# Performance work log

Hardware: AMD Instinct MI355X
Metric: run time of the kernel (lower is better)

The kernel has to match this reference:

```python
import jax, jax.numpy as jnp
import numpy as np

N = 4096     # num nodes
FEAT = 500   # knn attribute dim
HID = 512    # args.hid_dim
E = 65536    # edges (avg degree 16)
T = 8        # args.time -> euler steps with step_size=1


def setup_inputs() -> dict:
    key = jax.random.key(0)
    ks = jax.random.split(key, 10)
    knn = jax.random.normal(ks[0], (N, FEAT), jnp.float32)
    adj = jax.random.uniform(ks[1], (N, N), jnp.float32)
    norm_factor = jnp.ones((), jnp.float32)
    edge_index = jax.random.randint(ks[2], (2, E), 0, N, dtype=jnp.int32).astype(jnp.int64)
    edge_weight = jax.random.uniform(ks[3], (E,), jnp.float32)
    # AGCN params (init eye + small noise so math is non-trivial)
    w1 = jnp.eye(N, dtype=jnp.float32) + 0.01 * jax.random.normal(ks[4], (N, N), jnp.float32)
    w2 = jnp.eye(N, dtype=jnp.float32) + 0.01 * jax.random.normal(ks[5], (N, N), jnp.float32)
    # extractor: Linear(N, HID) then Linear(HID, HID), kaiming-normal (relu), zero bias
    W0 = jax.random.normal(ks[6], (HID, N), jnp.float32) * np.float32((2.0 / N) ** 0.5)
    b0 = jnp.zeros((HID,), jnp.float32)
    W1 = jax.random.normal(ks[7], (HID, HID), jnp.float32) * np.float32((2.0 / HID) ** 0.5)
    b1 = jnp.zeros((HID,), jnp.float32)
    # LaplacianODEFunc scalar params
    alpha_train = jnp.asarray(0.5, jnp.float32)
    beta_train = jnp.asarray(0.1, jnp.float32)
    return dict(knn=knn, adj=adj, norm_factor=norm_factor, w1=w1, w2=w2,
                W0=W0, b0=b0, W1=W1, b1=b1, edge_weight=edge_weight,
                alpha_train=alpha_train, beta_train=beta_train, edge_index=edge_index)


def _spmm(edge_index, edge_weight, x):
    # out[row] += w * x[col], row=edge_index[0], col=edge_index[1]
    msg = edge_weight[:, None] * x[edge_index[1]]          # [E, HID]
    return jax.ops.segment_sum(msg, edge_index[0], num_segments=x.shape[0])


def reference(knn, adj, norm_factor, w1, w2, W0, b0, W1, b1,
              edge_weight, alpha_train, beta_train, edge_index):
    # ---- AGCN ----
    H = (adj @ w1) @ adj.T                                  # [N, N]
    H = (H @ w2) @ knn                                      # [N, FEAT]
    embed = H @ H.T                                         # [N, N]
    norm = jnp.maximum(jnp.linalg.norm(embed, axis=1, keepdims=True), 1e-12)
    embed = embed / norm                                    # F.normalize(dim=1)
    # ---- extractor MLP (no activation in source; dropout=eval no-op) ----
    h = embed @ W0.T + b0                                   # [N, HID]
    h = h @ W1.T + b1                                       # [N, HID]
    # ---- ODE diffusion: dx/dt = sigmoid(a)*(Ax - x) + b*x0, explicit Euler dt=1 ----
    x0 = jax.lax.stop_gradient(h)
    alpha = jax.nn.sigmoid(alpha_train)

    def step(x, _):
        ax = _spmm(edge_index, edge_weight, x)
        return x + alpha * (ax - x) + beta_train * x0, None

    z_ode, _ = jax.lax.scan(step, h, None, length=T)
    z = jax.nn.relu(norm_factor * z_ode + h)
    z = (z - z.mean(0)) / jnp.std(z, ddof=1)                # torch std is unbiased
    return z
```

## Files before the change

kernel.cpp:

```cpp
#include <hip/hip_runtime.h>
#include <stdint.h>
#include <stddef.h>

typedef __bf16 bf16;
typedef __attribute__((ext_vector_type(8))) __bf16 bf16x8;
typedef __attribute__((ext_vector_type(4))) __bf16 bf16x4;
typedef __attribute__((ext_vector_type(4))) float f32x4;

#define NN 4096
#define HIDD 512
#define NE 65536

__device__ inline void gll16(const void* g, void* l) {
    __builtin_amdgcn_global_load_lds(
        (const __attribute__((address_space(1))) void*)g,
        (__attribute__((address_space(3))) void*)l, 16, 0, 0);
}

__global__ void cvt_f32_bf16(const float* __restrict__ in, bf16* __restrict__ out, int n) {
    int i = (blockIdx.x * 256 + threadIdx.x) * 4;
    if (i >= n) return;
    float4 v = *reinterpret_cast<const float4*>(in + i);
    bf16x4 o;
    o[0] = (bf16)v.x; o[1] = (bf16)v.y; o[2] = (bf16)v.z; o[3] = (bf16)v.w;
    *reinterpret_cast<bf16x4*>(out + i) = o;
}

__global__ void reduce_bf16_slices(const bf16* __restrict__ in, bf16* __restrict__ out,
                                   int n, int S) {
    int i = (blockIdx.x * 256 + threadIdx.x) * 8;
    if (i >= n) return;
    float acc[8] = {};
    for (int k = 0; k < S; ++k) {
        bf16x8 v = *reinterpret_cast<const bf16x8*>(in + (size_t)k * n + i);
#pragma unroll
        for (int j = 0; j < 8; ++j) acc[j] += (float)v[j];
    }
    bf16x8 o;
#pragma unroll
    for (int j = 0; j < 8; ++j) o[j] = (bf16)acc[j];
    *reinterpret_cast<bf16x8*>(out + i) = o;
}

__global__ void transpose_pad_f32(const float* __restrict__ in, bf16* __restrict__ out,
                                  int R, int C, int Cpad) {
    __shared__ bf16 tile[32][33];
    int c0 = blockIdx.x * 32, r0 = blockIdx.y * 32;
    int tx = threadIdx.x, ty = threadIdx.y;
    for (int i = ty; i < 32; i += 8) {
        int r = r0 + i, c = c0 + tx;
        bf16 v = (bf16)0.f;
        if (r < R && c < C) v = (bf16)in[(size_t)r * C + c];
        tile[i][tx] = v;
    }
    __syncthreads();
    for (int i = ty; i < 32; i += 8) {
        int oc = c0 + i, orow = r0 + tx;
        if (oc < Cpad && orow < R) out[(size_t)oc * R + orow] = tile[tx][i];
    }
}

__global__ void transpose_bf16(const bf16* __restrict__ in, bf16* __restrict__ out,
                               int R, int C) {
    __shared__ bf16 tile[32][33];
    int c0 = blockIdx.x * 32, r0 = blockIdx.y * 32;
    int tx = threadIdx.x, ty = threadIdx.y;
    for (int i = ty; i < 32; i += 8)
        tile[i][tx] = in[(size_t)(r0 + i) * C + c0 + tx];
    __syncthreads();
    for (int i = ty; i < 32; i += 8)
        out[(size_t)(c0 + i) * R + r0 + tx] = tile[tx][i];
}

template<int OMODE, bool HAS_BIAS, bool ROW_SCALE>
__global__ __launch_bounds__(256)
void gemm_nt(const bf16* __restrict__ A, const bf16* __restrict__ B,
             void* __restrict__ Cp, const float* __restrict__ bias,
             const float* __restrict__ rowscale, int M, int N, int K) {
    __shared__ __align__(16) bf16 As[128 * 32];
    __shared__ __align__(16) bf16 Bs[128 * 32];
    const int tid  = threadIdx.x;
    const int wave = tid >> 6;
    const int lane = tid & 63;
    const int m0 = blockIdx.y * 128, n0 = blockIdx.x * 128;
    const int lrow = lane >> 2;
    const int lcol = (lane & 3) * 8;
    const int c0 = wave * 2;
    const size_t arow0 = (size_t)(m0 + c0 * 16 + lrow) * K + lcol;
    const size_t arow1 = (size_t)(m0 + (c0 + 1) * 16 + lrow) * K + lcol;
    const size_t brow0 = (size_t)(n0 + c0 * 16 + lrow) * K + lcol;
    const size_t brow1 = (size_t)(n0 + (c0 + 1) * 16 + lrow) * K + lcol;
    bf16* asd0 = &As[c0 * 512];
    bf16* asd1 = &As[(c0 + 1) * 512];
    bf16* bsd0 = &Bs[c0 * 512];
    bf16* bsd1 = &Bs[(c0 + 1) * 512];

    f32x4 acc[4][4] = {};

    const int wm = (wave >> 1) * 64;
    const int wn = (wave & 1) * 64;
    const int fm = wm + (lane & 15);
    const int fn = wn + (lane & 15);
    const int fk = (lane >> 4) * 8;

    const int kper = K / gridDim.z;
    const int kz0 = blockIdx.z * kper;
    const int kz1 = kz0 + kper;

    for (int k0 = kz0; k0 < kz1; k0 += 32) {
        gll16(A + arow0 + k0, asd0);
        gll16(A + arow1 + k0, asd1);
        gll16(B + brow0 + k0, bsd0);
        gll16(B + brow1 + k0, bsd1);
        __syncthreads();
        bf16x8 af[4], bg[4];
#pragma unroll
        for (int i = 0; i < 4; ++i)
            af[i] = *reinterpret_cast<const bf16x8*>(&As[(fm + i * 16) * 32 + fk]);
#pragma unroll
        for (int j = 0; j < 4; ++j)
            bg[j] = *reinterpret_cast<const bf16x8*>(&Bs[(fn + j * 16) * 32 + fk]);
#pragma unroll
        for (int i = 0; i < 4; ++i)
#pragma unroll
            for (int j = 0; j < 4; ++j)
                acc[i][j] = __builtin_amdgcn_mfma_f32_16x16x32_bf16(af[i], bg[j], acc[i][j], 0, 0, 0);
        __syncthreads();
    }

    const int rbase = m0 + wm + (lane >> 4) * 4;
    const int cbase = n0 + wn + (lane & 15);
    float* outf = (float*)Cp + (size_t)blockIdx.z * M * N;
    bf16*  outb = (bf16*)Cp;
    bf16*  outp = (bf16*)Cp + (size_t)blockIdx.z * M * N;
#pragma unroll
    for (int i = 0; i < 4; ++i) {
#pragma unroll
        for (int j = 0; j < 4; ++j) {
            int col = cbase + j * 16;
            float bv = 0.f;
            if (HAS_BIAS) bv = bias[col];
#pragma unroll
            for (int r = 0; r < 4; ++r) {
                int row = rbase + i * 16 + r;
                float v = acc[i][j][r];
                if (ROW_SCALE) v *= rowscale[row];
                v += bv;
                if (OMODE == 0)      outf[(size_t)row * N + col] = v;
                else if (OMODE == 1) outb[(size_t)row * N + col] = (bf16)v;
                else                 outp[(size_t)row * N + col] = (bf16)v;
            }
        }
    }
}

__global__ void colnorm_part(const bf16* __restrict__ Ht, const float* __restrict__ Rf,
                             float* __restrict__ n2) {
    int i = blockIdx.x * 128 + threadIdx.x;
    int a0 = blockIdx.y * 64;
    float s = 0.f;
    for (int a = a0; a < a0 + 64; ++a)
        s += Rf[(size_t)a * NN + i] * (float)Ht[(size_t)a * NN + i];
    atomicAdd(&n2[i], s);
}

__global__ void colnorm_fin(const float* __restrict__ n2, float* __restrict__ inv) {
    int i = blockIdx.x * 256 + threadIdx.x;
    inv[i] = 1.f / fmaxf(sqrtf(n2[i]), 1e-12f);
}

__global__ void csr_count(const int* __restrict__ ei, int* __restrict__ cnt, int E) {
    int e = blockIdx.x * 256 + threadIdx.x;
    if (e < E) atomicAdd(&cnt[ei[e]], 1);
}

__global__ void scan_4096(const int* __restrict__ cnt, int* __restrict__ rs) {
    __shared__ int s[1024];
    int t = threadIdx.x;
    int b = t * 4;
    int a0 = cnt[b], a1 = cnt[b + 1], a2 = cnt[b + 2], a3 = cnt[b + 3];
    int tot = a0 + a1 + a2 + a3;
    s[t] = tot;
    __syncthreads();
    for (int off = 1; off < 1024; off <<= 1) {
        int v = (t >= off) ? s[t - off] : 0;
        __syncthreads();
        s[t] += v;
        __syncthreads();
    }
    int excl = s[t] - tot;
    rs[b] = excl; rs[b + 1] = excl + a0; rs[b + 2] = excl + a0 + a1; rs[b + 3] = excl + a0 + a1 + a2;
    if (t == 1023) rs[4096] = s[1023];
}

__global__ void csr_scatter(const int* __restrict__ ei, const float* __restrict__ ew,
                            int* __restrict__ cur, int* __restrict__ ccol,
                            float* __restrict__ cw, int E) {
    int e = blockIdx.x * 256 + threadIdx.x;
    if (e < E) {
        int r = ei[e];
        int p = atomicAdd(&cur[r], 1);
        ccol[p] = ei[E + e];
        cw[p] = ew[e];
    }
}

__global__ void ode_step_bf16(const bf16* __restrict__ xin, const bf16* __restrict__ x0,
                              bf16* __restrict__ xout, const int* __restrict__ rs,
                              const int* __restrict__ ccol, const float* __restrict__ cw,
                              const float* __restrict__ alpha_p, const float* __restrict__ beta_p) {
    int row = blockIdx.x * 4 + (threadIdx.x >> 6);
    int lane = threadIdx.x & 63;
    float alpha = 1.f / (1.f + expf(-alpha_p[0]));
    float beta = beta_p[0];
    const bf16x8* xin8 = (const bf16x8*)xin;
    float acc[8] = {};
    int p0 = rs[row], p1 = rs[row + 1];
    for (int p = p0; p < p1; ++p) {
        int c = ccol[p]; float w = cw[p];
        bf16x8 v = xin8[(size_t)c * 64 + lane];
#pragma unroll
        for (int j = 0; j < 8; ++j) acc[j] += w * (float)v[j];
    }
    bf16x8 xi = xin8[(size_t)row * 64 + lane];
    bf16x8 xz = ((const bf16x8*)x0)[(size_t)row * 64 + lane];
    bf16x8 r;
#pragma unroll
    for (int j = 0; j < 8; ++j) {
        float x = (float)xi[j];
        r[j] = (bf16)(x + alpha * (acc[j] - x) + beta * (float)xz[j]);
    }
    ((bf16x8*)xout)[(size_t)row * 64 + lane] = r;
}

__global__ void epi1(const bf16* __restrict__ x8, const bf16* __restrict__ h,
                     const float* __restrict__ nf_p, float* __restrict__ z,
                     float* __restrict__ colsum, float* __restrict__ gst) {
    __shared__ float r1[512], r2[512];
    int b = blockIdx.x, j = threadIdx.x;
    float nf = nf_p[0];
    float cp = 0.f, sq = 0.f;
    for (int i = 0; i < 8; ++i) {
        size_t idx = (size_t)(b * 8 + i) * HIDD + j;
        float v = nf * (float)x8[idx] + (float)h[idx];
        v = fmaxf(v, 0.f);
        z[idx] = v;
        cp += v; sq += v * v;
    }
    atomicAdd(&colsum[j], cp);
    r1[j] = cp; r2[j] = sq;
    __syncthreads();
    for (int off = 256; off > 0; off >>= 1) {
        if (j < off) { r1[j] += r1[j + off]; r2[j] += r2[j + off]; }
        __syncthreads();
    }
    if (j == 0) { atomicAdd(&gst[0], r1[0]); atomicAdd(&gst[1], r2[0]); }
}

__global__ void epi2(const float* __restrict__ z, const float* __restrict__ colsum,
                     const float* __restrict__ gst, float* __restrict__ out) {
    size_t idx = (size_t)blockIdx.x * 256 + threadIdx.x;
    int j = (int)(idx & (HIDD - 1));
    float n = (float)NN * (float)HIDD;
    float gmean = gst[0] / n;
    float var = (gst[1] - n * gmean * gmean) / (n - 1.f);
    float istd = rsqrtf(var);
    float mean = colsum[j] * (1.f / (float)NN);
    out[idx] = (z[idx] - mean) * istd;
}

extern "C" void kernel_launch(void* const* d_in, const int* in_sizes, int n_in,
                              void* d_out, int out_size, void* d_ws, size_t ws_size,
                              hipStream_t stream) {
    const float* knn  = (const float*)d_in[0];
    const float* adj  = (const float*)d_in[1];
    const float* nf   = (const float*)d_in[2];
    const float* w1   = (const float*)d_in[3];
    const float* w2   = (const float*)d_in[4];
    const float* W0   = (const float*)d_in[5];
    const float* b0   = (const float*)d_in[6];
    const float* W1   = (const float*)d_in[7];
    const float* b1   = (const float*)d_in[8];
    const float* ew   = (const float*)d_in[9];
    const float* alph = (const float*)d_in[10];
    const float* beta = (const float*)d_in[11];
    const int*   ei   = (const int*)d_in[12];

    char* w = (char*)d_ws;
    size_t off = 0;
    auto alloc = [&](size_t bytes) -> char* {
        char* p = w + off;
        off += (bytes + 255) & ~(size_t)255;
        return p;
    };
    const size_t SZ_NN  = (size_t)NN * NN * sizeof(bf16);
    const size_t SZ_TH  = (size_t)HIDD * NN * sizeof(bf16);
    bf16* Bar  = (bf16*)alloc(SZ_NN);
    bf16* Car  = (bf16*)alloc(SZ_NN);
    bf16* knnT = (bf16*)alloc(SZ_TH);
    bf16* tA   = (bf16*)alloc(SZ_TH);
    bf16* tB   = (bf16*)alloc(SZ_TH);
    float* tf  = (float*)alloc((size_t)16 * 1024 * 1024);
    bf16* Hm   = (bf16*)alloc(SZ_TH);
    bf16* Gb   = (bf16*)alloc((size_t)HIDD * HIDD * sizeof(bf16));
    bf16* M0tb = (bf16*)alloc((size_t)HIDD * HIDD * sizeof(bf16));
    bf16* h1b  = (bf16*)alloc((size_t)NN * HIDD * sizeof(bf16));
    bf16* hb   = (bf16*)alloc((size_t)NN * HIDD * sizeof(bf16));
    float* inv = (float*)alloc(NN * sizeof(float));
    float* n2  = (float*)alloc(NN * sizeof(float));
    int*  cnt  = (int*)alloc(NN * sizeof(int));
    int*  rs   = (int*)alloc((NN + 1) * sizeof(int));
    int*  cur  = (int*)alloc(NN * sizeof(int));
    int*  ccol = (int*)alloc(NE * sizeof(int));
    float* cw  = (float*)alloc(NE * sizeof(float));
    float* colsum = (float*)alloc(HIDD * sizeof(float));
    float* gst = (float*)alloc(2 * sizeof(float));
    bf16* tfb = (bf16*)tf;
    bf16* W1b = (bf16*)((char*)Car + 16 * 1024 * 1024);
    bf16* xA  = (bf16*)Car;
    bf16* xB  = (bf16*)Car + (size_t)NN * HIDD;
    (void)ws_size; (void)n_in; (void)in_sizes; (void)out_size;

    dim3 tb(32, 8);
    const int nTH = HIDD * NN;
    const int nHH = HIDD * HIDD;

    transpose_pad_f32<<<dim3(16, 128), tb, 0, stream>>>(knn, knnT, NN, 500, HIDD);
    cvt_f32_bf16<<<(NN * NN) / 1024, 256, 0, stream>>>(w2, Car, NN * NN);
    transpose_pad_f32<<<dim3(128, 128), tb, 0, stream>>>(adj, Bar, NN, NN, NN);

    gemm_nt<2, false, false><<<dim3(32, 4, 4), 256, 0, stream>>>(knnT, Car, tfb, nullptr, nullptr, HIDD, NN, NN);
    reduce_bf16_slices<<<nTH / 2048, 256, 0, stream>>>(tfb, tA, nTH, 4);
    gemm_nt<2, false, false><<<dim3(32, 4, 4), 256, 0, stream>>>(tA, Bar, tfb, nullptr, nullptr, HIDD, NN, NN);
    reduce_bf16_slices<<<nTH / 2048, 256, 0, stream>>>(tfb, tB, nTH, 4);
    cvt_f32_bf16<<<(NN * NN) / 1024, 256, 0, stream>>>(w1, Car, NN * NN);
    gemm_nt<2, false, false><<<dim3(32, 4, 4), 256, 0, stream>>>(tB, Car, tfb, nullptr, nullptr, HIDD, NN, NN);
    reduce_bf16_slices<<<nTH / 2048, 256, 0, stream>>>(tfb, tA, nTH, 4);
    cvt_f32_bf16<<<(NN * NN) / 1024, 256, 0, stream>>>(adj, Bar, NN * NN);
    gemm_nt<2, false, false><<<dim3(32, 4, 4), 256, 0, stream>>>(tA, Bar, tfb, nullptr, nullptr, HIDD, NN, NN);
    reduce_bf16_slices<<<nTH / 2048, 256, 0, stream>>>(tfb, tB, nTH, 4);

    transpose_bf16<<<dim3(128, 16), tb, 0, stream>>>(tB, Hm, HIDD, NN);

    gemm_nt<2, false, false><<<dim3(4, 4, 16), 256, 0, stream>>>(tB, tB, tfb, nullptr, nullptr, HIDD, HIDD, NN);
    reduce_bf16_slices<<<nHH / 2048, 256, 0, stream>>>(tfb, Gb, nHH, 16);

    gemm_nt<0, false, false><<<dim3(32, 4, 1), 256, 0, stream>>>(Gb, Hm, tf, nullptr, nullptr, HIDD, NN, HIDD);
    hipMemsetAsync(n2, 0, NN * sizeof(float), stream);
    colnorm_part<<<dim3(32, 8), 128, 0, stream>>>(tB, tf, n2);
    colnorm_fin<<<NN / 256, 256, 0, stream>>>(n2, inv);

    cvt_f32_bf16<<<(HIDD * NN) / 1024, 256, 0, stream>>>(W0, Car, HIDD * NN);
    gemm_nt<2, false, false><<<dim3(4, 4, 16), 256, 0, stream>>>(Car, tB, tfb, nullptr, nullptr, HIDD, HIDD, NN);
    reduce_bf16_slices<<<nHH / 2048, 256, 0, stream>>>(tfb, M0tb, nHH, 16);

    gemm_nt<1, true, true><<<dim3(4, 32, 1), 256, 0, stream>>>(Hm, M0tb, h1b, b0, inv, NN, HIDD, HIDD);
    cvt_f32_bf16<<<(HIDD * HIDD) / 1024, 256, 0, stream>>>(W1, W1b, HIDD * HIDD);
    gemm_nt<1, true, false><<<dim3(4, 32, 1), 256, 0, stream>>>(h1b, W1b, hb, b1, nullptr, NN, HIDD, HIDD);

    hipMemsetAsync(cnt, 0, NN * sizeof(int), stream);
    csr_count<<<NE / 256, 256, 0, stream>>>(ei, cnt, NE);
    scan_4096<<<1, 1024, 0, stream>>>(cnt, rs);
    hipMemcpyAsync(cur, rs, NN * sizeof(int), hipMemcpyDeviceToDevice, stream);
    csr_scatter<<<NE / 256, 256, 0, stream>>>(ei, ew, cur, ccol, cw, NE);

    const bf16* xi = hb;
    bf16* xo = xA;
    for (int s = 0; s < 8; ++s) {
        ode_step_bf16<<<NN / 4, 256, 0, stream>>>(xi, hb, xo, rs, ccol, cw, alph, beta);
        xi = xo;
        xo = (s % 2 == 0) ? xB : xA;
    }

    hipMemsetAsync(colsum, 0, HIDD * sizeof(float), stream);
    hipMemsetAsync(gst, 0, 2 * sizeof(float), stream);
    epi1<<<NN / 8, 512, 0, stream>>>(xB, hb, nf, tf, colsum, gst);
    epi2<<<(NN * HIDD) / 256, 256, 0, stream>>>(tf, colsum, gst, (float*)d_out);
}
```

Before: 676.0 us.

## Fold extractor weights into one GEMM, raise split-K, dual-output adj conversion

The transposed and plain bf16 copies of adj are now produced in a single pass, so the second fp32 conversion of adj is gone. Split-K depth is doubled for the large and Gram GEMMs, and the K=512 GEMMs are split into two slices. The two extractor linear layers are pre-multiplied into one 512x512 matrix (W1·M0) with a fused bias b1+W1·b0, which replaces one NxHID GEMM with a small HIDxHID GEMM. In exchange it adds more partial-sum traffic, extra reduce passes and an additional bf16 rounding of the combined weight.

```diff
diff --git a/kernel.cpp b/kernel.cpp
--- a/kernel.cpp
+++ b/kernel.cpp
@@ -58,6 +58,22 @@
         int oc = c0 + i, orow = r0 + tx;
         if (oc < Cpad && orow < R) out[(size_t)oc * R + orow] = tile[tx][i];
     }
+}
+
+__global__ void transpose_dual_f32(const float* __restrict__ in, bf16* __restrict__ outT,
+                                   bf16* __restrict__ outD, int Nn) {
+    __shared__ bf16 tile[32][33];
+    int c0 = blockIdx.x * 32, r0 = blockIdx.y * 32;
+    int tx = threadIdx.x, ty = threadIdx.y;
+    for (int i = ty; i < 32; i += 8) {
+        int r = r0 + i, c = c0 + tx;
+        bf16 v = (bf16)in[(size_t)r * Nn + c];
+        tile[i][tx] = v;
+        outD[(size_t)r * Nn + c] = v;
+    }
+    __syncthreads();
+    for (int i = ty; i < 32; i += 8)
+        outT[(size_t)(c0 + i) * Nn + r0 + tx] = tile[tx][i];
 }
 
 __global__ void transpose_bf16(const bf16* __restrict__ in, bf16* __restrict__ out,
@@ -158,15 +174,50 @@
                              float* __restrict__ n2) {
     int i = blockIdx.x * 128 + threadIdx.x;
     int a0 = blockIdx.y * 64;
+    const float* Rf2 = Rf + (size_t)HIDD * NN;
     float s = 0.f;
-    for (int a = a0; a < a0 + 64; ++a)
-        s += Rf[(size_t)a * NN + i] * (float)Ht[(size_t)a * NN + i];
+    for (int a = a0; a < a0 + 64; ++a) {
+        size_t idx = (size_t)a * NN + i;
+        s += (Rf[idx] + Rf2[idx]) * (float)Ht[idx];
+    }
     atomicAdd(&n2[i], s);
 }
 
 __global__ void colnorm_fin(const float* __restrict__ n2, float* __restrict__ inv) {
     int i = blockIdx.x * 256 + threadIdx.x;
     inv[i] = 1.f / fmaxf(sqrtf(n2[i]), 1e-12f);
+}
+
+__global__ void bias_fuse(const float* __restrict__ W1, const float* __restrict__ b0,
+                          const float* __restrict__ b1, float* __restrict__ bp) {
+    int row = blockIdx.x * 4 + (threadIdx.x >> 6);
+    int lane = threadIdx.x & 63;
+    const float4* wr = (const float4*)(W1 + (size_t)row * HIDD);
+    const float4* bz = (const float4*)b0;
+    float s = 0.f;
+#pragma unroll
+    for (int j = 0; j < 2; ++j) {
+        float4 a = wr[lane * 2 + j], b = bz[lane * 2 + j];
+        s += a.x * b.x + a.y * b.y + a.z * b.z + a.w * b.w;
+    }
+    for (int off = 32; off; off >>= 1) s += __shfl_down(s, off);
+    if (lane == 0) bp[row] = b1[row] + s;
+}
+
+__global__ void reduce2_scale_bias(const bf16* __restrict__ p, bf16* __restrict__ out,
+                                   const float* __restrict__ inv, const float* __restrict__ bp) {
+    int i = (blockIdx.x * 256 + threadIdx.x) * 8;
+    const int n = NN * HIDD;
+    bf16x8 a = *reinterpret_cast<const bf16x8*>(p + i);
+    bf16x8 b = *reinterpret_cast<const bf16x8*>(p + n + i);
+    int row = i >> 9;
+    int col = i & (HIDD - 1);
+    float sc = inv[row];
+    bf16x8 o;
+#pragma unroll
+    for (int j = 0; j < 8; ++j)
+        o[j] = (bf16)(((float)a[j] + (float)b[j]) * sc + bp[col + j]);
+    *reinterpret_cast<bf16x8*>(out + i) = o;
 }
 
 __global__ void csr_count(const int* __restrict__ ei, int* __restrict__ cnt, int E) {
@@ -297,14 +348,15 @@
     const size_t SZ_TH  = (size_t)HIDD * NN * sizeof(bf16);
     bf16* Bar  = (bf16*)alloc(SZ_NN);
     bf16* Car  = (bf16*)alloc(SZ_NN);
+    bf16* Adjb = (bf16*)alloc(SZ_NN);
     bf16* knnT = (bf16*)alloc(SZ_TH);
     bf16* tA   = (bf16*)alloc(SZ_TH);
     bf16* tB   = (bf16*)alloc(SZ_TH);
-    float* tf  = (float*)alloc((size_t)16 * 1024 * 1024);
+    float* tf  = (float*)alloc((size_t)32 * 1024 * 1024);
     bf16* Hm   = (bf16*)alloc(SZ_TH);
     bf16* Gb   = (bf16*)alloc((size_t)HIDD * HIDD * sizeof(bf16));
-    bf16* M0tb = (bf16*)alloc((size_t)HIDD * HIDD * sizeof(bf16));
-    bf16* h1b  = (bf16*)alloc((size_t)NN * HIDD * sizeof(bf16));
+    bf16* M0b  = (bf16*)alloc((size_t)HIDD * HIDD * sizeof(bf16));
+    bf16* Qtb  = (bf16*)alloc((size_t)HIDD * HIDD * sizeof(bf16));
     bf16* hb   = (bf16*)alloc((size_t)NN * HIDD * sizeof(bf16));
     float* inv = (float*)alloc(NN * sizeof(float));
     float* n2  = (float*)alloc(NN * sizeof(float));
@@ -315,6 +367,7 @@
     float* cw  = (float*)alloc(NE * sizeof(float));
     float* colsum = (float*)alloc(HIDD * sizeof(float));
     float* gst = (float*)alloc(2 * sizeof(float));
+    float* bp  = (float*)alloc(HIDD * sizeof(float));
     bf16* tfb = (bf16*)tf;
     bf16* W1b = (bf16*)((char*)Car + 16 * 1024 * 1024);
     bf16* xA  = (bf16*)Car;
@@ -327,36 +380,40 @@
 
     transpose_pad_f32<<<dim3(16, 128), tb, 0, stream>>>(knn, knnT, NN, 500, HIDD);
     cvt_f32_bf16<<<(NN * NN) / 1024, 256, 0, stream>>>(w2, Car, NN * NN);
-    transpose_pad_f32<<<dim3(128, 128), tb, 0, stream>>>(adj, Bar, NN, NN, NN);
-
-    gemm_nt<2, false, false><<<dim3(32, 4, 4), 256, 0, stream>>>(knnT, Car, tfb, nullptr, nullptr, HIDD, NN, NN);
-    reduce_bf16_slices<<<nTH / 2048, 256, 0, stream>>>(tfb, tA, nTH, 4);
-    gemm_nt<2, false, false><<<dim3(32, 4, 4), 256, 0, stream>>>(tA, Bar, tfb, nullptr, nullptr, HIDD, NN, NN);
-    reduce_bf16_slices<<<nTH / 2048, 256, 0, stream>>>(tfb, tB, nTH, 4);
+    transpose_dual_f32<<<dim3(128, 128), tb, 0, stream>>>(adj, Bar, Adjb, NN);
+
+    gemm_nt<2, false, false><<<dim3(32, 4, 8), 256, 0, stream>>>(knnT, Car, tfb, nullptr, nullptr, HIDD, NN, NN);
+    reduce_bf16_slices<<<nTH / 2048, 256, 0, stream>>>(tfb, tA, nTH, 8);
+    gemm_nt<2, false, false><<<dim3(32, 4, 8), 256, 0, stream>>>(tA, Bar, tfb, nullptr, nullptr, HIDD, NN, NN);
+    reduce_bf16_slices<<<nTH / 2048, 256, 0, stream>>>(tfb, tB, nTH, 8);
     cvt_f32_bf16<<<(NN * NN) / 1024, 256, 0, stream>>>(w1, Car, NN * NN);
-    gemm_nt<2, false, false><<<dim3(32, 4, 4), 256, 0, stream>>>(tB, Car, tfb, nullptr, nullptr, HIDD, NN, NN);
-    reduce_bf16_slices<<<nTH / 2048, 256, 0, stream>>>(tfb, tA, nTH, 4);
-    cvt_f32_bf16<<<(NN * NN) / 1024, 256, 0, stream>>>(adj, Bar, NN * NN);
-    gemm_nt<2, false, false><<<dim3(32, 4, 4), 256, 0, stream>>>(tA, Bar, tfb, nullptr, nullptr, HIDD, NN, NN);
-    reduce_bf16_slices<<<nTH / 2048, 256, 0, stream>>>(tfb, tB, nTH, 4);
+    gemm_nt<2, false, false><<<dim3(32, 4, 8), 256, 0, stream>>>(tB, Car, tfb, nullptr, nullptr, HIDD, NN, NN);
+    reduce_bf16_slices<<<nTH / 2048, 256, 0, stream>>>(tfb, tA, nTH, 8);
+    gemm_nt<2, false, false><<<dim3(32, 4, 8), 256, 0, stream>>>(tA, Adjb, tfb, nullptr, nullptr, HIDD, NN, NN);
+    reduce_bf16_slices<<<nTH / 2048, 256, 0, stream>>>(tfb, tB, nTH, 8);
 
     transpose_bf16<<<dim3(128, 16), tb, 0, stream>>>(tB, Hm, HIDD, NN);
 
-    gemm_nt<2, false, false><<<dim3(4, 4, 16), 256, 0, stream>>>(tB, tB, tfb, nullptr, nullptr, HIDD, HIDD, NN);
-    reduce_bf16_slices<<<nHH / 2048, 256, 0, stream>>>(tfb, Gb, nHH, 16);
-
-    gemm_nt<0, false, false><<<dim3(32, 4, 1), 256, 0, stream>>>(Gb, Hm, tf, nullptr, nullptr, HIDD, NN, HIDD);
+    gemm_nt<2, false, false><<<dim3(4, 4, 32), 256, 0, stream>>>(tB, tB, tfb, nullptr, nullptr, HIDD, HIDD, NN);
+    reduce_bf16_slices<<<nHH / 2048, 256, 0, stream>>>(tfb, Gb, nHH, 32);
+
+    gemm_nt<0, false, false><<<dim3(32, 4, 2), 256, 0, stream>>>(Gb, Hm, tf, nullptr, nullptr, HIDD, NN, HIDD);
     hipMemsetAsync(n2, 0, NN * sizeof(float), stream);
     colnorm_part<<<dim3(32, 8), 128, 0, stream>>>(tB, tf, n2);
     colnorm_fin<<<NN / 256, 256, 0, stream>>>(n2, inv);
 
     cvt_f32_bf16<<<(HIDD * NN) / 1024, 256, 0, stream>>>(W0, Car, HIDD * NN);
-    gemm_nt<2, false, false><<<dim3(4, 4, 16), 256, 0, stream>>>(Car, tB, tfb, nullptr, nullptr, HIDD, HIDD, NN);
-    reduce_bf16_slices<<<nHH / 2048, 256, 0, stream>>>(tfb, M0tb, nHH, 16);
-
-    gemm_nt<1, true, true><<<dim3(4, 32, 1), 256, 0, stream>>>(Hm, M0tb, h1b, b0, inv, NN, HIDD, HIDD);
+    gemm_nt<2, false, false><<<dim3(4, 4, 32), 256, 0, stream>>>(tB, Car, tfb, nullptr, nullptr, HIDD, HIDD, NN);
+    reduce_bf16_slices<<<nHH / 2048, 256, 0, stream>>>(tfb, M0b, nHH, 32);
+
     cvt_f32_bf16<<<(HIDD * HIDD) / 1024, 256, 0, stream>>>(W1, W1b, HIDD * HIDD);
-    gemm_nt<1, true, false><<<dim3(4, 32, 1), 256, 0, stream>>>(h1b, W1b, hb, b1, nullptr, NN, HIDD, HIDD);
+    gemm_nt<2, false, false><<<dim3(4, 4, 8), 256, 0, stream>>>(W1b, M0b, tfb, nullptr, nullptr, HIDD, HIDD, HIDD);
+    reduce_bf16_slices<<<nHH / 2048, 256, 0, stream>>>(tfb, Qtb, nHH, 8);
+
+    bias_fuse<<<128, 256, 0, stream>>>(W1, b0, b1, bp);
+
+    gemm_nt<2, false, false><<<dim3(4, 32, 2), 256, 0, stream>>>(Hm, Qtb, tfb, nullptr, nullptr, NN, HIDD, HIDD);
+    reduce2_scale_bias<<<(NN * HIDD) / 2048, 256, 0, stream>>>(tfb, hb, inv, bp);
 
     hipMemsetAsync(cnt, 0, NN * sizeof(int), stream);
     csr_count<<<NE / 256, 256, 0, stream>>>(ei, cnt, NE);
```

After: 694.1 us. +2.7%, slower.
